# Optimization experiments

Measured on AMD Instinct MI355X. Metric: run time of the kernel, lower is better.

## Reference

```python
import jax, jax.numpy as jnp
import numpy as np

P_SIZE = 5
NUM_HEAD = 8
GN_EPS = 1e-5
LRELU_SLOPE = 0.2


def conv1x1(w, x, b=None):
    # w: [out_c, in_c], x: [n, in_c, h, w]
    y = jnp.einsum('oc,nchw->nohw', w, x)
    if b is not None:
        y = y + b[None, :, None, None]
    return y


def bilinear_sample(feat, sx, sy):
    """grid_sample(mode='bilinear', padding_mode='zeros', align_corners=True).
    With align_corners=True the normalize/denormalize round-trip in
    deformation_grid/grid_sample is the identity, so sx,sy are raw pixel coords.
    feat: [n,c,H,W]; sx,sy: [n,P,H,W] -> out [n,c,P,H,W]."""
    n, c, H, W = feat.shape
    x0 = jnp.floor(sx)
    y0 = jnp.floor(sy)
    x1 = x0 + 1.0
    y1 = y0 + 1.0
    wx1 = sx - x0
    wx0 = 1.0 - wx1
    wy1 = sy - y0
    wy0 = 1.0 - wy1
    feat_flat = feat.reshape(n, c, H * W)

    def corner(xi, yi, wgt):
        valid = (xi >= 0) & (xi <= W - 1) & (yi >= 0) & (yi <= H - 1)
        xc = jnp.clip(xi, 0, W - 1).astype(jnp.int32)
        yc = jnp.clip(yi, 0, H - 1).astype(jnp.int32)
        idx = (yc * W + xc).reshape(n, -1)                      # [n, P*H*W]
        g = jnp.take_along_axis(feat_flat, idx[:, None, :], axis=2)  # [n,c,P*H*W]
        g = g.reshape(n, c, xi.shape[1], H, W)                  # [n,c,P,H,W]
        wm = (wgt * valid.astype(feat.dtype))[:, None]          # [n,1,P,H,W]
        return g * wm

    return (corner(x0, y0, wx0 * wy0) + corner(x1, y0, wx1 * wy0)
            + corner(x0, y1, wx0 * wy1) + corner(x1, y1, wx1 * wy1))


def sample_coords(deform_field, p_size):
    # deform_field: [n,2,h,w] -> absolute pixel coords sx, sy: [n, p^2, h, w]
    n, _, h, w = deform_field.shape
    padding = (p_size - 1) // 2
    shift = jnp.arange(p_size, dtype=deform_field.dtype) - padding
    shift_y, shift_x = jnp.meshgrid(shift, shift, indexing='ij')  # [p,p]
    shift_y = shift_y.reshape(-1, 1, 1)  # [p^2,1,1]
    shift_x = shift_x.reshape(-1, 1, 1)
    gy = jnp.arange(h, dtype=deform_field.dtype)[:, None]  # [h,1]
    gx = jnp.arange(w, dtype=deform_field.dtype)[None, :]  # [1,w]
    sx = gx[None] + shift_x + deform_field[:, None, 0]     # [n,p^2,h,w]
    sy = gy[None] + shift_y + deform_field[:, None, 1]
    return sx, sy


def setup_inputs() -> dict:
    key = jax.random.key(0)
    ks = jax.random.split(key, 12)
    n, c, h, w = 2, 128, 96, 96
    hid = 256
    s = 0.05
    return {
        'query': jax.random.normal(ks[0], (n, c, h, w), jnp.float32),
        'key': jax.random.normal(ks[1], (n, c, h, w), jnp.float32),
        'value': jax.random.normal(ks[2], (n, c, h, w), jnp.float32),
        'deform_field': jax.random.normal(ks[3], (n, 2, h, w), jnp.float32) * 2.0,
        'w_q': jax.random.normal(ks[4], (c, c), jnp.float32) * s,
        'w_k': jax.random.normal(ks[5], (c, c), jnp.float32) * s,
        'w_v': jax.random.normal(ks[6], (c, c), jnp.float32) * s,
        'w_fc': jax.random.normal(ks[7], (c, c), jnp.float32) * s,
        'mlp_w1': jax.random.normal(ks[8], (hid, c), jnp.float32) * s,
        'mlp_b1': jnp.zeros((hid,), jnp.float32),
        'mlp_w2': jax.random.normal(ks[9], (c, hid), jnp.float32) * s,
        'mlp_b2': jnp.zeros((c,), jnp.float32),
        'gn_gamma': jnp.ones((c,), jnp.float32),
        'gn_beta': jnp.zeros((c,), jnp.float32),
    }


def reference(query, key, value, deform_field, w_q, w_k, w_v, w_fc,
              mlp_w1, mlp_b1, mlp_w2, mlp_b2, gn_gamma, gn_beta):
    p2 = P_SIZE * P_SIZE
    n, c, h, w = query.shape
    d_k = c // NUM_HEAD

    q = conv1x1(w_q, query)   # [n,c,h,w]
    k = conv1x1(w_k, key)
    v = conv1x1(w_v, value)

    # deformable window sampling of keys/values
    sx, sy = sample_coords(deform_field, P_SIZE)      # [n,p^2,h,w]
    k_s = bilinear_sample(k, sx, sy)                  # [n,c,p^2,h,w]
    v_s = bilinear_sample(v, sx, sy)

    # split heads
    q = q.reshape(n, NUM_HEAD, d_k, h, w)
    k_s = k_s.reshape(n, NUM_HEAD, d_k, p2, h, w)
    v_s = v_s.reshape(n, NUM_HEAD, d_k, p2, h, w)

    scale = 1.0 / jnp.sqrt(jnp.asarray(d_k, q.dtype))
    attn = jnp.einsum('nedyx,nedpyx->neyxp', q * scale, k_s)   # [n,head,h,w,p^2]
    attn = jax.nn.softmax(attn, axis=-1)
    out = jnp.einsum('neyxp,nedpyx->nedyx', attn, v_s)          # [n,head,d_v,h,w]
    out = out.reshape(n, c, h, w)
    out = conv1x1(w_fc, out)

    # conv-MLP residual
    hdn = conv1x1(mlp_w1, out, mlp_b1)
    hdn = jnp.where(hdn >= 0, hdn, LRELU_SLOPE * hdn)
    out = out + conv1x1(mlp_w2, hdn, mlp_b2)

    # GroupNorm(1, feat_dim): normalize over (C,H,W) per sample, per-channel affine
    mean = jnp.mean(out, axis=(1, 2, 3), keepdims=True)
    var = jnp.mean(jnp.square(out - mean), axis=(1, 2, 3), keepdims=True)
    out = (out - mean) * jax.lax.rsqrt(var + GN_EPS)
    out = out * gn_gamma[None, :, None, None] + gn_beta[None, :, None, None]
    return out
```

## Files before the change

kernel.cpp:

```cpp
#include <hip/hip_runtime.h>
#include <cstddef>

constexpr int Cc = 128;
constexpr int Hh = 96;
constexpr int Ww = 96;
constexpr int HW = Hh * Ww;
constexpr int Nn = 2;

typedef __attribute__((ext_vector_type(2))) _Float16 f16x2;
typedef __attribute__((ext_vector_type(4))) _Float16 f16x4;
typedef __attribute__((ext_vector_type(8))) _Float16 f16x8;
typedef __attribute__((ext_vector_type(4))) float f32x4;

__device__ __forceinline__ float fdot2(f16x2 a, f16x2 b, float c) {
#if defined(__has_builtin) && __has_builtin(__builtin_amdgcn_fdot2)
    return __builtin_amdgcn_fdot2(a, b, c, false);
#else
    return (float)a[0] * (float)b[0] + (float)a[1] * (float)b[1] + c;
#endif
}

__global__ void __launch_bounds__(256)
wcvt_k(const float* __restrict__ wq, const float* __restrict__ wk,
       const float* __restrict__ wv, const float* __restrict__ wfc,
       const float* __restrict__ w1, const float* __restrict__ w2,
       _Float16* __restrict__ dst)
{
    const int h0 = (blockIdx.x * 256 + threadIdx.x) * 8;
    const float* src; int off, K;
    if (h0 < 16384)      { src = wq;  off = h0;          K = 128; }
    else if (h0 < 32768) { src = wk;  off = h0 - 16384;  K = 128; }
    else if (h0 < 49152) { src = wv;  off = h0 - 32768;  K = 128; }
    else if (h0 < 65536) { src = wfc; off = h0 - 49152;  K = 128; }
    else if (h0 < 98304) { src = w1;  off = h0 - 65536;  K = 128; }
    else                 { src = w2;  off = h0 - 98304;  K = 256; }
    const int fid  = off >> 3;
    const int lane = fid & 63;
    const int n16  = lane & 15, quad = lane >> 4;
    const int t2   = fid >> 6;
    const int kcN  = K / 32;
    const int kc   = t2 % kcN;
    const int mt   = t2 / kcN;
    const int row  = mt * 16 + n16;
    const int col  = kc * 32 + quad * 8;
    const float* s = src + (size_t)row * K + col;
    const float4 a = *(const float4*)s;
    const float4 b = *(const float4*)(s + 4);
    f16x8 h = {(_Float16)a.x, (_Float16)a.y, (_Float16)a.z, (_Float16)a.w,
               (_Float16)b.x, (_Float16)b.y, (_Float16)b.z, (_Float16)b.w};
    *(f16x8*)&dst[h0] = h;
}

__global__ void __launch_bounds__(128)
kv_k(const float* __restrict__ Xk, const float* __restrict__ Xv,
     const _Float16* __restrict__ w16,
     _Float16* __restrict__ k16, _Float16* __restrict__ v16)
{
    const int t  = blockIdx.y;
    const int p0 = blockIdx.x * 64;
    const int z  = blockIdx.z;
    const float* X = (t == 0) ? Xk : Xv;
    _Float16* Y    = (t == 0) ? k16 : v16;
    const _Float16* W = w16 + 16384 + (size_t)t * 16384;

    __shared__ _Float16 xl[128][72];
    const int tid = threadIdx.x;
    {
        const int px4 = (tid & 15) * 4, kg = tid >> 4;
        const float* Xz = X + (size_t)z * Cc * HW + p0 + px4;
#pragma unroll
        for (int kk = 0; kk < 16; ++kk) {
            const int k = kk * 8 + kg;
            float4 a = *(const float4*)&Xz[(size_t)k * HW];
            f16x4 h = {(_Float16)a.x, (_Float16)a.y, (_Float16)a.z, (_Float16)a.w};
            *(f16x4*)&xl[k][px4] = h;
        }
    }
    __syncthreads();

    const int w = tid >> 6, lane = tid & 63;
    const int n16 = lane & 15, quad = lane >> 4;
    const int pw = w * 32;

    f16x8 A[2][4];
#pragma unroll
    for (int mi = 0; mi < 2; ++mi) {
        const int px = pw + mi * 16 + n16;
#pragma unroll
        for (int kcid = 0; kcid < 4; ++kcid) {
            f16x8 av;
#pragma unroll
            for (int j = 0; j < 8; ++j) av[j] = xl[kcid * 32 + quad * 8 + j][px];
            A[mi][kcid] = av;
        }
    }

#pragma unroll
    for (int half = 0; half < 2; ++half) {
        const int oc0 = half * 64;
        f32x4 acc[2][4];
#pragma unroll
        for (int mi = 0; mi < 2; ++mi)
#pragma unroll
            for (int ni = 0; ni < 4; ++ni) acc[mi][ni] = (f32x4)0.f;

#pragma unroll
        for (int kcid = 0; kcid < 4; ++kcid) {
            f16x8 B[4];
#pragma unroll
            for (int ni = 0; ni < 4; ++ni)
                B[ni] = *(const f16x8*)&W[(((half * 4 + ni) * 4 + kcid) * 64 + lane) * 8];
#pragma unroll
            for (int mi = 0; mi < 2; ++mi)
#pragma unroll
                for (int ni = 0; ni < 4; ++ni)
                    acc[mi][ni] = __builtin_amdgcn_mfma_f32_16x16x32_f16(
                        A[mi][kcid], B[ni], acc[mi][ni], 0, 0, 0);
        }

#pragma unroll
        for (int mi = 0; mi < 2; ++mi)
#pragma unroll
            for (int r = 0; r < 4; ++r) {
                const int pix = p0 + pw + mi * 16 + quad * 4 + r;
                const size_t base = ((size_t)z * HW + pix) * Cc + oc0;
#pragma unroll
                for (int ni = 0; ni < 4; ++ni)
                    Y[base + ni * 16 + n16] = (_Float16)acc[mi][ni][r];
            }
    }
}

__global__ void __launch_bounds__(256)
qaf_k(const float* __restrict__ Xq, const _Float16* __restrict__ w16,
      const _Float16* __restrict__ k16, const _Float16* __restrict__ v16,
      const float* __restrict__ df, const float* __restrict__ b1,
      const float* __restrict__ b2, _Float16* __restrict__ y2,
      float* __restrict__ pb)
{
    __shared__ __align__(16) _Float16 xl[128][18];
    __shared__ __align__(16) _Float16 ql[16][140];
    __shared__ __align__(16) _Float16 y1l[16][140];
    __shared__ __align__(16) _Float16 hl[16][264];
    __shared__ float red[8];

    const int z  = blockIdx.z;
    const int bx = blockIdx.x;
    const int ti = (bx & 7) * 72 + (bx >> 3);
    const int p0 = ti * 16;
    const int tid = threadIdx.x, w = tid >> 6, lane = tid & 63;
    const int n16 = lane & 15, quad = lane >> 4;

    {
        const int px4 = (tid & 3) * 4, k0 = tid >> 2;
        const float* Xz = Xq + (size_t)z * Cc * HW + p0 + px4;
#pragma unroll
        for (int kk = 0; kk < 2; ++kk) {
            const int k = kk * 64 + k0;
            float4 a = *(const float4*)&Xz[(size_t)k * HW];
            f16x2 lo = {(_Float16)a.x, (_Float16)a.y};
            f16x2 hi = {(_Float16)a.z, (_Float16)a.w};
            *(f16x2*)&xl[k][px4]     = lo;
            *(f16x2*)&xl[k][px4 + 2] = hi;
        }
    }
    __syncthreads();

    {
        f32x4 qa[2];
        qa[0] = (f32x4)0.f; qa[1] = (f32x4)0.f;
#pragma unroll
        for (int kc = 0; kc < 4; ++kc) {
            f16x8 A;
#pragma unroll
            for (int j = 0; j < 8; ++j) A[j] = xl[kc * 32 + quad * 8 + j][n16];
#pragma unroll
            for (int ni = 0; ni < 2; ++ni) {
                const f16x8 B = *(const f16x8*)&w16[(((w * 2 + ni) * 4 + kc) * 64 + lane) * 8];
                qa[ni] = __builtin_amdgcn_mfma_f32_16x16x32_f16(A, B, qa[ni], 0, 0, 0);
            }
        }
#pragma unroll
        for (int ni = 0; ni < 2; ++ni)
#pragma unroll
            for (int r = 0; r < 4; ++r)
                ql[quad * 4 + r][w * 32 + ni * 16 + n16] = (_Float16)qa[ni][r];
    }
    __syncthreads();

    {
        const int lpx = w * 4 + (lane >> 4);
        const int pix = p0 + lpx;
        const int y = pix / Ww, x = pix - y * Ww;
        const int co = n16 * 8;

        const float dx = df[((size_t)z * 2 + 0) * HW + pix];
        const float dy = df[((size_t)z * 2 + 1) * HW + pix];
        const float flx = floorf(dx), fly = floorf(dy);
        const int bxp = x - 2 + (int)flx;
        const int byp = y - 2 + (int)fly;
        const float wx1 = dx - flx, wx0 = 1.f - wx1;
        const float wy1 = dy - fly, wy0 = 1.f - wy1;
        const float s00 = wy0 * wx0 * 0.25f, s01 = wy0 * wx1 * 0.25f,
                    s10 = wy1 * wx0 * 0.25f, s11 = wy1 * wx1 * 0.25f;

        const f16x8 qv8 = *(const f16x8*)&ql[lpx][co];
        const f16x2 q0 = {qv8[0], qv8[1]}, q1 = {qv8[2], qv8[3]},
                    q2 = {qv8[4], qv8[5]}, q3 = {qv8[6], qv8[7]};

        const _Float16* kp = k16 + ((size_t)z * HW) * Cc + co;
        const _Float16* vp = v16 + ((size_t)z * HW) * Cc + co;

        const bool inb = (bxp >= 0) & (byp >= 0) & (bxp <= Ww - 6) & (byp <= Hh - 6);
        const int allin = __all(inb);

        float qk[36];
        if (allin) {
            const _Float16* kr = kp + (size_t)(byp * Ww + bxp) * Cc;
#pragma unroll
            for (int r = 0; r < 6; ++r) {
#pragma unroll
                for (int c = 0; c < 6; ++c) {
                    const f16x8 kv = *(const f16x8*)&kr[c * Cc];
                    f16x2 k0 = {kv[0], kv[1]}, k1 = {kv[2], kv[3]};
                    f16x2 k2 = {kv[4], kv[5]}, k3 = {kv[6], kv[7]};
                    float d = fdot2(q0, k0, 0.f);
                    d = fdot2(q1, k1, d);
                    d = fdot2(q2, k2, d);
                    d = fdot2(q3, k3, d);
                    qk[r * 6 + c] = d;
                }
                kr += Ww * Cc;
            }
        } else {
#pragma unroll
            for (int r = 0; r < 6; ++r) {
                const int yr = byp + r;
                const bool rv = (yr >= 0) & (yr < Hh);
                const int yc = min(max(yr, 0), Hh - 1);
                const _Float16* kr = kp + (size_t)(yc * Ww) * Cc;
#pragma unroll
                for (int c = 0; c < 6; ++c) {
                    const int xc = bxp + c;
                    const bool cv = rv & (xc >= 0) & (xc < Ww);
                    const int xcc = min(max(xc, 0), Ww - 1);
                    const f16x8 kv = *(const f16x8*)&kr[xcc * Cc];
                    f16x2 k0 = {kv[0], kv[1]}, k1 = {kv[2], kv[3]};
                    f16x2 k2 = {kv[4], kv[5]}, k3 = {kv[6], kv[7]};
                    float d = fdot2(q0, k0, 0.f);
                    d = fdot2(q1, k1, d);
                    d = fdot2(q2, k2, d);
                    d = fdot2(q3, k3, d);
                    qk[r * 6 + c] = cv ? d : 0.f;
                }
            }
        }

        float a[25];
#pragma unroll
        for (int py = 0; py < 5; ++py)
#pragma unroll
            for (int px = 0; px < 5; ++px) {
                float tv = s00 * qk[py * 6 + px];
                tv = fmaf(s01, qk[py * 6 + px + 1], tv);
                tv = fmaf(s10, qk[(py + 1) * 6 + px], tv);
                tv = fmaf(s11, qk[(py + 1) * 6 + px + 1], tv);
                a[py * 5 + px] = tv;
            }
#pragma unroll
        for (int i = 0; i < 25; ++i) a[i] += __shfl_xor(a[i], 1, 64);

        float mx = a[0];
#pragma unroll
        for (int i = 1; i < 25; ++i) mx = fmaxf(mx, a[i]);
        float ssum = 0.f;
#pragma unroll
        for (int i = 0; i < 25; ++i) { a[i] = __expf(a[i] - mx); ssum += a[i]; }
        const float inv = 1.f / ssum;

        float tmp[6][5];
#pragma unroll
        for (int r = 0; r < 6; ++r)
#pragma unroll
            for (int px = 0; px < 5; ++px) {
                float tv = 0.f;
                if (r < 5)  tv = a[r * 5 + px] * wy0;
                if (r >= 1) tv = fmaf(a[(r - 1) * 5 + px], wy1, tv);
                tmp[r][px] = tv;
            }
        float wsum[36];
#pragma unroll
        for (int r = 0; r < 6; ++r)
#pragma unroll
            for (int c = 0; c < 6; ++c) {
                float tv = 0.f;
                if (c < 5)  tv = tmp[r][c] * wx0;
                if (c >= 1) tv = fmaf(tmp[r][c - 1], wx1, tv);
                wsum[r * 6 + c] = tv;
            }

        float o[8] = {0.f, 0.f, 0.f, 0.f, 0.f, 0.f, 0.f, 0.f};
        if (allin) {
            const _Float16* vr = vp + (size_t)(byp * Ww + bxp) * Cc;
#pragma unroll
            for (int r = 0; r < 6; ++r) {
#pragma unroll
                for (int c = 0; c < 6; ++c) {
                    const f16x8 vv = *(const f16x8*)&vr[c * Cc];
                    const float wgt = wsum[r * 6 + c];
#pragma unroll
                    for (int j = 0; j < 8; ++j)
                        o[j] = fmaf(wgt, (float)vv[j], o[j]);
                }
                vr += Ww * Cc;
            }
        } else {
#pragma unroll
            for (int r = 0; r < 6; ++r) {
                const int yr = byp + r;
                const bool rv = (yr >= 0) & (yr < Hh);
                const int yc = min(max(yr, 0), Hh - 1);
                const _Float16* vr = vp + (size_t)(yc * Ww) * Cc;
#pragma unroll
                for (int c = 0; c < 6; ++c) {
                    const int xc = bxp + c;
                    const bool cv = rv & (xc >= 0) & (xc < Ww);
                    const int xcc = min(max(xc, 0), Ww - 1);
                    const f16x8 vv = *(const f16x8*)&vr[xcc * Cc];
                    const float wgt = cv ? wsum[r * 6 + c] : 0.f;
#pragma unroll
                    for (int j = 0; j < 8; ++j)
                        o[j] = fmaf(wgt, (float)vv[j], o[j]);
                }
            }
        }

        f16x8 ov;
#pragma unroll
        for (int j = 0; j < 8; ++j) ov[j] = (_Float16)(o[j] * inv);
        *(f16x8*)&ql[lpx][co] = ov;
    }
    __syncthreads();

    const _Float16* Wfc = w16 + 49152;
    const _Float16* W1  = w16 + 65536;
    const _Float16* W2  = w16 + 98304;

    f32x4 acc1[2];
    acc1[0] = (f32x4)0.f; acc1[1] = (f32x4)0.f;
#pragma unroll
    for (int kc = 0; kc < 4; ++kc) {
        const f16x8 A = *(const f16x8*)&ql[n16][kc * 32 + quad * 8];
#pragma unroll
        for (int ni = 0; ni < 2; ++ni) {
            const f16x8 B = *(const f16x8*)&Wfc[(((w * 2 + ni) * 4 + kc) * 64 + lane) * 8];
            acc1[ni] = __builtin_amdgcn_mfma_f32_16x16x32_f16(A, B, acc1[ni], 0, 0, 0);
        }
    }
#pragma unroll
    for (int ni = 0; ni < 2; ++ni)
#pragma unroll
        for (int r = 0; r < 4; ++r)
            y1l[quad * 4 + r][w * 32 + ni * 16 + n16] = (_Float16)acc1[ni][r];
    __syncthreads();

    {
        f32x4 acc2[4];
#pragma unroll
        for (int ni = 0; ni < 4; ++ni) acc2[ni] = (f32x4)0.f;
#pragma unroll
        for (int kc = 0; kc < 4; ++kc) {
            const f16x8 A = *(const f16x8*)&y1l[n16][kc * 32 + quad * 8];
#pragma unroll
            for (int ni = 0; ni < 4; ++ni) {
                const f16x8 B = *(const f16x8*)&W1[(((w * 4 + ni) * 4 + kc) * 64 + lane) * 8];
                acc2[ni] = __builtin_amdgcn_mfma_f32_16x16x32_f16(A, B, acc2[ni], 0, 0, 0);
            }
        }
        float b1v[4];
#pragma unroll
        for (int ni = 0; ni < 4; ++ni) b1v[ni] = b1[w * 64 + ni * 16 + n16];
#pragma unroll
        for (int ni = 0; ni < 4; ++ni)
#pragma unroll
            for (int r = 0; r < 4; ++r) {
                float tv = acc2[ni][r] + b1v[ni];
                tv = tv >= 0.f ? tv : 0.2f * tv;
                hl[quad * 4 + r][w * 64 + ni * 16 + n16] = (_Float16)tv;
            }
    }
    __syncthreads();

    f32x4 acc3[2];
    acc3[0] = (f32x4)0.f; acc3[1] = (f32x4)0.f;
#pragma unroll
    for (int kc = 0; kc < 8; ++kc) {
        const f16x8 A = *(const f16x8*)&hl[n16][kc * 32 + quad * 8];
#pragma unroll
        for (int ni = 0; ni < 2; ++ni) {
            const f16x8 B = *(const f16x8*)&W2[(((w * 2 + ni) * 8 + kc) * 64 + lane) * 8];
            acc3[ni] = __builtin_amdgcn_mfma_f32_16x16x32_f16(A, B, acc3[ni], 0, 0, 0);
        }
    }

    float b2v[2];
#pragma unroll
    for (int ni = 0; ni < 2; ++ni) b2v[ni] = b2[w * 32 + ni * 16 + n16];

    float lsum = 0.f, lsq = 0.f;
#pragma unroll
    for (int ni = 0; ni < 2; ++ni)
#pragma unroll
        for (int r = 0; r < 4; ++r) {
            const int pix = p0 + quad * 4 + r;
            const float tv = acc3[ni][r] + b2v[ni] + acc1[ni][r];
            lsum += tv; lsq += tv * tv;
            y2[((size_t)z * HW + pix) * Cc + w * 32 + ni * 16 + n16] = (_Float16)tv;
        }

#pragma unroll
    for (int m = 1; m < 64; m <<= 1) {
        lsum += __shfl_xor(lsum, m, 64);
        lsq  += __shfl_xor(lsq,  m, 64);
    }
    if (lane == 0) { red[w * 2] = lsum; red[w * 2 + 1] = lsq; }
    __syncthreads();
    if (tid == 0) {
        float S = 0.f, Q = 0.f;
#pragma unroll
        for (int i = 0; i < 4; ++i) { S += red[i * 2]; Q += red[i * 2 + 1]; }
        const int bid = z * (HW / 16) + bx;
        pb[bid * 2 + 0] = S;
        pb[bid * 2 + 1] = Q;
    }
}

__global__ void __launch_bounds__(256)
gn_k(const _Float16* __restrict__ y2, const float* __restrict__ pb,
     const float* __restrict__ gamma, const float* __restrict__ beta,
     float* __restrict__ out, const int nPerZ)
{
    __shared__ float t[32][68];
    __shared__ float redm[8];
    __shared__ float stats[2];
    const int z = blockIdx.z, c0 = blockIdx.y * 32, p0 = blockIdx.x * 64;
    const int tid = threadIdx.x;

    {
        float s = 0.f, qq = 0.f;
        for (int p = tid; p < nPerZ; p += 256) {
            s  += pb[(z * nPerZ + p) * 2 + 0];
            qq += pb[(z * nPerZ + p) * 2 + 1];
        }
#pragma unroll
        for (int m = 1; m < 64; m <<= 1) {
            s  += __shfl_xor(s,  m, 64);
            qq += __shfl_xor(qq, m, 64);
        }
        if ((tid & 63) == 0) {
            redm[(tid >> 6) * 2]     = s;
            redm[(tid >> 6) * 2 + 1] = qq;
        }
    }
    {
        const int px = tid >> 2, cq = tid & 3;
        const f16x8 a = *(const f16x8*)&y2[((size_t)z * HW + p0 + px) * Cc + c0 + cq * 8];
#pragma unroll
        for (int j = 0; j < 8; ++j) t[cq * 8 + j][px] = (float)a[j];
    }
    __syncthreads();
    if (tid == 0) {
        const float invN = 1.f / (float)(Cc * HW);
        const float S = redm[0] + redm[2] + redm[4] + redm[6];
        const float Q = redm[1] + redm[3] + redm[5] + redm[7];
        const float mean = S * invN;
        const float var  = fmaf(-mean, mean, Q * invN);
        stats[0] = mean;
        stats[1] = rsqrtf(var + 1e-5f);
    }
    __syncthreads();
    {
        const float mean = stats[0], rs = stats[1];
        const int c = tid >> 3, pq = tid & 7;
        const float g = gamma[c0 + c] * rs, be = beta[c0 + c];
        float4 o1, o2;
        o1.x = fmaf(t[c][pq * 8 + 0] - mean, g, be);
        o1.y = fmaf(t[c][pq * 8 + 1] - mean, g, be);
        o1.z = fmaf(t[c][pq * 8 + 2] - mean, g, be);
        o1.w = fmaf(t[c][pq * 8 + 3] - mean, g, be);
        o2.x = fmaf(t[c][pq * 8 + 4] - mean, g, be);
        o2.y = fmaf(t[c][pq * 8 + 5] - mean, g, be);
        o2.z = fmaf(t[c][pq * 8 + 6] - mean, g, be);
        o2.w = fmaf(t[c][pq * 8 + 7] - mean, g, be);
        float* dst = &out[((size_t)z * Cc + c0 + c) * HW + p0 + pq * 8];
        *(float4*)dst = o1;
        *(float4*)(dst + 4) = o2;
    }
}

extern "C" void kernel_launch(void* const* d_in, const int* in_sizes, int n_in,
                              void* d_out, int out_size, void* d_ws, size_t ws_size,
                              hipStream_t stream)
{
    const float* query  = (const float*)d_in[0];
    const float* key    = (const float*)d_in[1];
    const float* value  = (const float*)d_in[2];
    const float* deform = (const float*)d_in[3];
    const float* w_q    = (const float*)d_in[4];
    const float* w_k    = (const float*)d_in[5];
    const float* w_v    = (const float*)d_in[6];
    const float* w_fc   = (const float*)d_in[7];
    const float* mlp_w1 = (const float*)d_in[8];
    const float* mlp_b1 = (const float*)d_in[9];
    const float* mlp_w2 = (const float*)d_in[10];
    const float* mlp_b2 = (const float*)d_in[11];
    const float* gn_g   = (const float*)d_in[12];
    const float* gn_b   = (const float*)d_in[13];
    float* out = (float*)d_out;

    char* wsb = (char*)d_ws;
    _Float16* w16 = (_Float16*)wsb;
    float* pb   = (float*)(wsb + 262144);
    _Float16* T = (_Float16*)(wsb + 524288);
    const size_t S16 = (size_t)Nn * HW * Cc;
    _Float16* k16  = T;
    _Float16* v16  = T + S16;
    _Float16* y2h  = T + 2 * S16;

    wcvt_k<<<dim3(64), dim3(256), 0, stream>>>(
        w_q, w_k, w_v, w_fc, mlp_w1, mlp_w2, w16);

    kv_k<<<dim3(HW / 64, 2, Nn), dim3(128), 0, stream>>>(
        key, value, w16, k16, v16);

    qaf_k<<<dim3(HW / 16, 1, Nn), dim3(256), 0, stream>>>(
        query, w16, k16, v16, deform, mlp_b1, mlp_b2, y2h, pb);

    gn_k<<<dim3(HW / 64, Cc / 32, Nn), dim3(256), 0, stream>>>(
        y2h, pb, gn_g, gn_b, out, HW / 16);
}
```

Measured before the change: 141.7 us.

## Halve pixels per block in fused attention kernel, spread channels over more lanes

The fused query/attention/MLP kernel now processes 8 pixels per block instead of 16, doubling the grid. Each pixel's channel slice is split across 32 lanes with 4 channels each instead of 16 lanes with 8, so a 4-lane shuffle reduction is used. The QK bilinear combination is streamed row by row, and the V weights are computed on the fly, to cut register pressure. Launch bounds now request 6 waves for occupancy. The cost is that MFMA tiles are half-empty (the upper 8 rows are zero-padded), so more work is wasted and more blocks are launched.

New measurement: 186.7 us. +31.8%, slower.

```diff
diff --git a/kernel.cpp b/kernel.cpp
--- a/kernel.cpp
+++ b/kernel.cpp
@@ -131,38 +131,39 @@
     }
 }
 
-__global__ void __launch_bounds__(256)
+__global__ void __launch_bounds__(256, 6)
 qaf_k(const float* __restrict__ Xq, const _Float16* __restrict__ w16,
       const _Float16* __restrict__ k16, const _Float16* __restrict__ v16,
       const float* __restrict__ df, const float* __restrict__ b1,
       const float* __restrict__ b2, _Float16* __restrict__ y2,
       float* __restrict__ pb)
 {
-    __shared__ __align__(16) _Float16 xl[128][18];
-    __shared__ __align__(16) _Float16 ql[16][140];
-    __shared__ __align__(16) _Float16 y1l[16][140];
+    __shared__ __align__(16) _Float16 xl[128][16];
+    __shared__ __align__(16) _Float16 ql[16][136];
+    __shared__ __align__(16) _Float16 y1l[16][136];
     __shared__ __align__(16) _Float16 hl[16][264];
     __shared__ float red[8];
 
     const int z  = blockIdx.z;
     const int bx = blockIdx.x;
-    const int ti = (bx & 7) * 72 + (bx >> 3);
-    const int p0 = ti * 16;
+    const int ti = (bx & 7) * 144 + (bx >> 3);
+    const int p0 = ti * 8;
     const int tid = threadIdx.x, w = tid >> 6, lane = tid & 63;
     const int n16 = lane & 15, quad = lane >> 4;
 
     {
-        const int px4 = (tid & 3) * 4, k0 = tid >> 2;
+#pragma unroll
+        for (int i = tid; i < 1024; i += 256) xl[i >> 3][8 + (i & 7)] = (_Float16)0.f;
+    }
+
+    {
+        const int px4 = (tid & 1) * 4, k0 = tid >> 1;
         const float* Xz = Xq + (size_t)z * Cc * HW + p0 + px4;
-#pragma unroll
-        for (int kk = 0; kk < 2; ++kk) {
-            const int k = kk * 64 + k0;
-            float4 a = *(const float4*)&Xz[(size_t)k * HW];
-            f16x2 lo = {(_Float16)a.x, (_Float16)a.y};
-            f16x2 hi = {(_Float16)a.z, (_Float16)a.w};
-            *(f16x2*)&xl[k][px4]     = lo;
-            *(f16x2*)&xl[k][px4 + 2] = hi;
-        }
+        float4 a = *(const float4*)&Xz[(size_t)k0 * HW];
+        f16x2 lo = {(_Float16)a.x, (_Float16)a.y};
+        f16x2 hi = {(_Float16)a.z, (_Float16)a.w};
+        *(f16x2*)&xl[k0][px4]     = lo;
+        *(f16x2*)&xl[k0][px4 + 2] = hi;
     }
     __syncthreads();
 
@@ -189,10 +190,11 @@
     __syncthreads();
 
     {
-        const int lpx = w * 4 + (lane >> 4);
+        const int lpx = w * 2 + (lane >> 5);
         const int pix = p0 + lpx;
         const int y = pix / Ww, x = pix - y * Ww;
-        const int co = n16 * 8;
+        const int cl = lane & 31;
+        const int co = cl * 4;
 
         const float dx = df[((size_t)z * 2 + 0) * HW + pix];
         const float dy = df[((size_t)z * 2 + 1) * HW + pix];
@@ -204,9 +206,8 @@
         const float s00 = wy0 * wx0 * 0.25f, s01 = wy0 * wx1 * 0.25f,
                     s10 = wy1 * wx0 * 0.25f, s11 = wy1 * wx1 * 0.25f;
 
-        const f16x8 qv8 = *(const f16x8*)&ql[lpx][co];
-        const f16x2 q0 = {qv8[0], qv8[1]}, q1 = {qv8[2], qv8[3]},
-                    q2 = {qv8[4], qv8[5]}, q3 = {qv8[6], qv8[7]};
+        const f16x4 qv4 = *(const f16x4*)&ql[lpx][co];
+        const f16x2 q0 = {qv4[0], qv4[1]}, q1 = {qv4[2], qv4[3]};
 
         const _Float16* kp = k16 + ((size_t)z * HW) * Cc + co;
         const _Float16* vp = v16 + ((size_t)z * HW) * Cc + co;
@@ -214,22 +215,31 @@
         const bool inb = (bxp >= 0) & (byp >= 0) & (bxp <= Ww - 6) & (byp <= Hh - 6);
         const int allin = __all(inb);
 
-        float qk[36];
+        float a[25];
+        float qkP[6], qkC[6];
         if (allin) {
             const _Float16* kr = kp + (size_t)(byp * Ww + bxp) * Cc;
 #pragma unroll
             for (int r = 0; r < 6; ++r) {
 #pragma unroll
                 for (int c = 0; c < 6; ++c) {
-                    const f16x8 kv = *(const f16x8*)&kr[c * Cc];
+                    const f16x4 kv = *(const f16x4*)&kr[c * Cc];
                     f16x2 k0 = {kv[0], kv[1]}, k1 = {kv[2], kv[3]};
-                    f16x2 k2 = {kv[4], kv[5]}, k3 = {kv[6], kv[7]};
                     float d = fdot2(q0, k0, 0.f);
-                    d = fdot2(q1, k1, d);
-                    d = fdot2(q2, k2, d);
-                    d = fdot2(q3, k3, d);
-                    qk[r * 6 + c] = d;
-                }
+                    qkC[c] = fdot2(q1, k1, d);
+                }
+                if (r >= 1) {
+#pragma unroll
+                    for (int px = 0; px < 5; ++px) {
+                        float tv = s00 * qkP[px];
+                        tv = fmaf(s01, qkP[px + 1], tv);
+                        tv = fmaf(s10, qkC[px], tv);
+                        tv = fmaf(s11, qkC[px + 1], tv);
+                        a[(r - 1) * 5 + px] = tv;
+                    }
+                }
+#pragma unroll
+                for (int c = 0; c < 6; ++c) qkP[c] = qkC[c];
                 kr += Ww * Cc;
             }
         } else {
@@ -244,31 +254,32 @@
                     const int xc = bxp + c;
                     const bool cv = rv & (xc >= 0) & (xc < Ww);
                     const int xcc = min(max(xc, 0), Ww - 1);
-                    const f16x8 kv = *(const f16x8*)&kr[xcc * Cc];
+                    const f16x4 kv = *(const f16x4*)&kr[xcc * Cc];
                     f16x2 k0 = {kv[0], kv[1]}, k1 = {kv[2], kv[3]};
-                    f16x2 k2 = {kv[4], kv[5]}, k3 = {kv[6], kv[7]};
                     float d = fdot2(q0, k0, 0.f);
                     d = fdot2(q1, k1, d);
-                    d = fdot2(q2, k2, d);
-                    d = fdot2(q3, k3, d);
-                    qk[r * 6 + c] = cv ? d : 0.f;
-                }
-            }
-        }
-
-        float a[25];
-#pragma unroll
-        for (int py = 0; py < 5; ++py)
-#pragma unroll
-            for (int px = 0; px < 5; ++px) {
-                float tv = s00 * qk[py * 6 + px];
-                tv = fmaf(s01, qk[py * 6 + px + 1], tv);
-                tv = fmaf(s10, qk[(py + 1) * 6 + px], tv);
-                tv = fmaf(s11, qk[(py + 1) * 6 + px + 1], tv);
-                a[py * 5 + px] = tv;
-            }
-#pragma unroll
-        for (int i = 0; i < 25; ++i) a[i] += __shfl_xor(a[i], 1, 64);
+                    qkC[c] = cv ? d : 0.f;
+                }
+                if (r >= 1) {
+#pragma unroll
+                    for (int px = 0; px < 5; ++px) {
+                        float tv = s00 * qkP[px];
+                        tv = fmaf(s01, qkP[px + 1], tv);
+                        tv = fmaf(s10, qkC[px], tv);
+                        tv = fmaf(s11, qkC[px + 1], tv);
+                        a[(r - 1) * 5 + px] = tv;
+                    }
+                }
+#pragma unroll
+                for (int c = 0; c < 6; ++c) qkP[c] = qkC[c];
+            }
+        }
+
+#pragma unroll
+        for (int i = 0; i < 25; ++i) {
+            a[i] += __shfl_xor(a[i], 1, 64);
+            a[i] += __shfl_xor(a[i], 2, 64);
+        }
 
         float mx = a[0];
 #pragma unroll
@@ -278,38 +289,27 @@
         for (int i = 0; i < 25; ++i) { a[i] = __expf(a[i] - mx); ssum += a[i]; }
         const float inv = 1.f / ssum;
 
-        float tmp[6][5];
-#pragma unroll
-        for (int r = 0; r < 6; ++r)
-#pragma unroll
-            for (int px = 0; px < 5; ++px) {
-                float tv = 0.f;
-                if (r < 5)  tv = a[r * 5 + px] * wy0;
-                if (r >= 1) tv = fmaf(a[(r - 1) * 5 + px], wy1, tv);
-                tmp[r][px] = tv;
-            }
-        float wsum[36];
-#pragma unroll
-        for (int r = 0; r < 6; ++r)
-#pragma unroll
-            for (int c = 0; c < 6; ++c) {
-                float tv = 0.f;
-                if (c < 5)  tv = tmp[r][c] * wx0;
-                if (c >= 1) tv = fmaf(tmp[r][c - 1], wx1, tv);
-                wsum[r * 6 + c] = tv;
-            }
-
-        float o[8] = {0.f, 0.f, 0.f, 0.f, 0.f, 0.f, 0.f, 0.f};
+        float o[4] = {0.f, 0.f, 0.f, 0.f};
         if (allin) {
             const _Float16* vr = vp + (size_t)(byp * Ww + bxp) * Cc;
 #pragma unroll
             for (int r = 0; r < 6; ++r) {
+                float tr[5];
+#pragma unroll
+                for (int px = 0; px < 5; ++px) {
+                    float tv = 0.f;
+                    if (r < 5)  tv = a[r * 5 + px] * wy0;
+                    if (r >= 1) tv = fmaf(a[(r - 1) * 5 + px], wy1, tv);
+                    tr[px] = tv;
+                }
 #pragma unroll
                 for (int c = 0; c < 6; ++c) {
-                    const f16x8 vv = *(const f16x8*)&vr[c * Cc];
-                    const float wgt = wsum[r * 6 + c];
-#pragma unroll
-                    for (int j = 0; j < 8; ++j)
+                    float wgt = 0.f;
+                    if (c < 5)  wgt = tr[c] * wx0;
+                    if (c >= 1) wgt = fmaf(tr[c - 1], wx1, wgt);
+                    const f16x4 vv = *(const f16x4*)&vr[c * Cc];
+#pragma unroll
+                    for (int j = 0; j < 4; ++j)
                         o[j] = fmaf(wgt, (float)vv[j], o[j]);
                 }
                 vr += Ww * Cc;
@@ -317,6 +317,14 @@
         } else {
 #pragma unroll
             for (int r = 0; r < 6; ++r) {
+                float tr[5];
+#pragma unroll
+                for (int px = 0; px < 5; ++px) {
+                    float tv = 0.f;
+                    if (r < 5)  tv = a[r * 5 + px] * wy0;
+                    if (r >= 1) tv = fmaf(a[(r - 1) * 5 + px], wy1, tv);
+                    tr[px] = tv;
+                }
                 const int yr = byp + r;
                 const bool rv = (yr >= 0) & (yr < Hh);
                 const int yc = min(max(yr, 0), Hh - 1);
@@ -326,19 +334,22 @@
                     const int xc = bxp + c;
                     const bool cv = rv & (xc >= 0) & (xc < Ww);
                     const int xcc = min(max(xc, 0), Ww - 1);
-                    const f16x8 vv = *(const f16x8*)&vr[xcc * Cc];
-                    const float wgt = cv ? wsum[r * 6 + c] : 0.f;
-#pragma unroll
-                    for (int j = 0; j < 8; ++j)
+                    float wgt = 0.f;
+                    if (c < 5)  wgt = tr[c] * wx0;
+                    if (c >= 1) wgt = fmaf(tr[c - 1], wx1, wgt);
+                    wgt = cv ? wgt : 0.f;
+                    const f16x4 vv = *(const f16x4*)&vr[xcc * Cc];
+#pragma unroll
+                    for (int j = 0; j < 4; ++j)
                         o[j] = fmaf(wgt, (float)vv[j], o[j]);
                 }
             }
         }
 
-        f16x8 ov;
-#pragma unroll
-        for (int j = 0; j < 8; ++j) ov[j] = (_Float16)(o[j] * inv);
-        *(f16x8*)&ql[lpx][co] = ov;
+        f16x4 ov;
+#pragma unroll
+        for (int j = 0; j < 4; ++j) ov[j] = (_Float16)(o[j] * inv);
+        *(f16x4*)&ql[lpx][co] = ov;
     }
     __syncthreads();
 
@@ -408,15 +419,17 @@
     for (int ni = 0; ni < 2; ++ni) b2v[ni] = b2[w * 32 + ni * 16 + n16];
 
     float lsum = 0.f, lsq = 0.f;
-#pragma unroll
-    for (int ni = 0; ni < 2; ++ni)
-#pragma unroll
-        for (int r = 0; r < 4; ++r) {
-            const int pix = p0 + quad * 4 + r;
-            const float tv = acc3[ni][r] + b2v[ni] + acc1[ni][r];
-            lsum += tv; lsq += tv * tv;
-            y2[((size_t)z * HW + pix) * Cc + w * 32 + ni * 16 + n16] = (_Float16)tv;
-        }
+    if (quad < 2) {
+#pragma unroll
+        for (int ni = 0; ni < 2; ++ni)
+#pragma unroll
+            for (int r = 0; r < 4; ++r) {
+                const int pix = p0 + quad * 4 + r;
+                const float tv = acc3[ni][r] + b2v[ni] + acc1[ni][r];
+                lsum += tv; lsq += tv * tv;
+                y2[((size_t)z * HW + pix) * Cc + w * 32 + ni * 16 + n16] = (_Float16)tv;
+            }
+    }
 
 #pragma unroll
     for (int m = 1; m < 64; m <<= 1) {
@@ -429,7 +442,7 @@
         float S = 0.f, Q = 0.f;
 #pragma unroll
         for (int i = 0; i < 4; ++i) { S += red[i * 2]; Q += red[i * 2 + 1]; }
-        const int bid = z * (HW / 16) + bx;
+        const int bid = z * (HW / 8) + bx;
         pb[bid * 2 + 0] = S;
         pb[bid * 2 + 1] = Q;
     }
@@ -533,9 +546,9 @@
     kv_k<<<dim3(HW / 64, 2, Nn), dim3(128), 0, stream>>>(
         key, value, w16, k16, v16);
 
-    qaf_k<<<dim3(HW / 16, 1, Nn), dim3(256), 0, stream>>>(
+    qaf_k<<<dim3(HW / 8, 1, Nn), dim3(256), 0, stream>>>(
         query, w16, k16, v16, deform, mlp_b1, mlp_b2, y2h, pb);
 
     gn_k<<<dim3(HW / 64, Cc / 32, Nn), dim3(256), 0, stream>>>(
-        y2h, pb, gn_g, gn_b, out, HW / 16);
+        y2h, pb, gn_g, gn_b, out, HW / 8);
 }
```
